# Optimization experiments

Hardware: AMD Instinct MI355X
Metric: run time of the kernel (lower is better)

Reference implementation:

```python
import jax, jax.numpy as jnp
import numpy as np

N = 10000           # nodes
E = 160000          # edges
MUL = 128           # multiplicity of each irrep (128x0e + 128x1o)
EDGE_FEAT = 8       # radial embedding dim
AVG_NUM_NEIGHBORS = 16.0
MLP_IN = MUL + MUL + EDGE_FEAT + 1  # 265
NUM_W = 4 * MUL     # irreps_mid num_irreps = 256x0e + 256x1o -> 512 path weights
SQ3 = float(np.sqrt(3.0))


def setup_inputs() -> dict:
    key = jax.random.key(0)
    ks = jax.random.split(key, 16)
    node_feats = jax.random.normal(ks[0], (N, 4 * MUL), dtype=jnp.float32)  # [N,512] = 128x0e ++ 128x1o
    edge_attrs = jax.random.normal(ks[1], (E, 4), dtype=jnp.float32)        # 1x0e ++ 1x1o
    edge_feats = jax.random.normal(ks[2], (E, EDGE_FEAT), dtype=jnp.float32)
    lengths = jax.random.uniform(ks[3], (E, 1), dtype=jnp.float32)
    edge_index = jax.random.randint(ks[4], (2, E), 0, N, dtype=jnp.int32)
    # e3nn Linear weights (stored unit-variance; forward applies 1/sqrt(fan_in))
    W_scalar = jax.random.normal(ks[5], (MUL, MUL), dtype=jnp.float32)
    W_up0 = jax.random.normal(ks[6], (MUL, MUL), dtype=jnp.float32)
    W_up1 = jax.random.normal(ks[7], (MUL, MUL), dtype=jnp.float32)
    # conv_tp_weights MLP (flax Dense: fan-scaled init, bias on first two layers)
    W1 = jax.random.normal(ks[8], (MLP_IN, MUL), dtype=jnp.float32) / np.sqrt(MLP_IN)
    b1 = jnp.zeros((MUL,), dtype=jnp.float32)
    W2 = jax.random.normal(ks[9], (MUL, MUL), dtype=jnp.float32) / np.sqrt(MUL)
    b2 = jnp.zeros((MUL,), dtype=jnp.float32)
    W3 = jax.random.normal(ks[10], (MUL, NUM_W), dtype=jnp.float32) / np.sqrt(MUL)
    # final e3nn Linear: 256x0e+256x1o -> 128x0e+128x1o
    Wout0 = jax.random.normal(ks[11], (2 * MUL, MUL), dtype=jnp.float32)
    Wout1 = jax.random.normal(ks[12], (2 * MUL, MUL), dtype=jnp.float32)
    return {"node_feats": node_feats, "edge_attrs": edge_attrs, "edge_feats": edge_feats,
            "lengths": lengths, "edge_index": edge_index, "W_scalar": W_scalar,
            "W_up0": W_up0, "W_up1": W_up1, "W1": W1, "b1": b1, "W2": W2, "b2": b2,
            "W3": W3, "Wout0": Wout0, "Wout1": Wout1}


def reference(node_feats, edge_attrs, edge_feats, lengths, edge_index,
              W_scalar, W_up0, W_up1, W1, b1, W2, b2, W3, Wout0, Wout1):
    n = node_feats.shape[0]
    inv = 1.0 / np.sqrt(MUL)
    x0 = node_feats[:, :MUL]                       # [N,128]   0e
    x1 = node_feats[:, MUL:].reshape(n, MUL, 3)    # [N,128,3] 1o

    # linear_scalar: only 0e->0e path survives
    scalars = (x0 @ W_scalar) * inv                # [N,128]
    # linear_up: per-irrep channel mixing
    h0 = (x0 @ W_up0) * inv                        # [N,128]
    h1 = jnp.einsum('nmi,mo->noi', x1, W_up1) * inv  # [N,128,3]

    sender, receiver = edge_index[0], edge_index[1]

    # conv_tp_weights MLP
    mlp_in = jnp.concatenate([scalars[sender], scalars[receiver], edge_feats, lengths], axis=-1)
    h = jax.nn.silu(mlp_in @ W1 + b1)
    h = jax.nn.silu(h @ W2 + b2)
    tpw = h @ W3                                   # [E,512]

    xs0 = h0[sender]                               # [E,128]
    xs1 = h1[sender]                               # [E,128,3]
    y0 = edge_attrs[:, 0:1]                        # [E,1]  0e
    y1 = edge_attrs[:, 1:4]                        # [E,3]  1o

    # CG tensor product (component normalization), filtered to {0e,1o}; sorted order:
    # 0e block = [0e*0e->0e, 1o*1o->0e], 1o block = [0e*1o->1o, 1o*0e->1o]
    mA = xs0 * y0                                       # [E,128]   0e
    mD = (xs1 * y1[:, None, :]).sum(-1) / SQ3           # [E,128]   0e
    mB = xs0[:, :, None] * y1[:, None, :]               # [E,128,3] 1o
    mC = xs1 * y0[:, :, None]                           # [E,128,3] 1o

    # per-irrep path weights (one scalar per irrep channel)
    wA, wD = tpw[:, :MUL], tpw[:, MUL:2 * MUL]
    wB, wC = tpw[:, 2 * MUL:3 * MUL], tpw[:, 3 * MUL:]

    m0 = jnp.concatenate([mA * wA, mD * wD], axis=1)                          # [E,256]
    m1 = jnp.concatenate([mB * wB[:, :, None], mC * wC[:, :, None]], axis=1)  # [E,256,3]

    # scatter-sum aggregation to receivers
    agg0 = jax.ops.segment_sum(m0, receiver, num_segments=n)  # [N,256]
    agg1 = jax.ops.segment_sum(m1, receiver, num_segments=n)  # [N,256,3]

    # final e3nn Linear + / avg_num_neighbors
    scale = 1.0 / (np.sqrt(2 * MUL) * AVG_NUM_NEIGHBORS)
    out0 = (agg0 @ Wout0) * scale                             # [N,128]
    out1 = jnp.einsum('nmi,mo->noi', agg1, Wout1) * scale     # [N,128,3]

    # reshape_irreps: [N, mul, sum(ir dims)] = [N,128,4]
    return jnp.concatenate([out0[:, :, None], out1], axis=-1)
```

## Files before the change

### kernel.cpp

```cpp
#include <hip/hip_runtime.h>
#include <hip/hip_bf16.h>

#define NN 10000
#define NE 160000
#define TILE 32
#define A1S 296
#define A2S 136

typedef __attribute__((ext_vector_type(8))) short short8;
typedef __attribute__((ext_vector_type(4))) float f32x4;

__device__ __forceinline__ float silu_f(float x) { return x / (1.0f + __expf(-x)); }
__device__ __forceinline__ unsigned short bf16u(float v) {
    __hip_bfloat16 b = __float2bfloat16(v);
    return *reinterpret_cast<unsigned short*>(&b);
}
__device__ __forceinline__ short8 pack8(float4 a, float4 b) {
    short8 r;
    r[0]=(short)bf16u(a.x); r[1]=(short)bf16u(a.y); r[2]=(short)bf16u(a.z); r[3]=(short)bf16u(a.w);
    r[4]=(short)bf16u(b.x); r[5]=(short)bf16u(b.y); r[6]=(short)bf16u(b.z); r[7]=(short)bf16u(b.w);
    return r;
}
__device__ __forceinline__ void lds_barrier() {
    asm volatile("s_waitcnt lgkmcnt(0)" ::: "memory");
    __builtin_amdgcn_s_barrier();
    asm volatile("" ::: "memory");
}

#define OFF_W1  0
#define OFF_W2  36864
#define OFF_W3  53248
#define OFF_WSC 118784
#define OFF_WU0 135168
#define OFF_WU1 151552
#define OFF_WO0 167936
#define OFF_WO1 200704
#define WP_TOTAL 233472

__global__ __launch_bounds__(256) void convert_weights(
    const float* __restrict__ W1, const float* __restrict__ W2,
    const float* __restrict__ W3, const float* __restrict__ Wsc,
    const float* __restrict__ Wu0, const float* __restrict__ Wu1,
    const float* __restrict__ Wo0, const float* __restrict__ Wo1,
    unsigned short* __restrict__ wp,
    const int* __restrict__ edge_index, int* __restrict__ deg)
{
    int idx = blockIdx.x * 256 + threadIdx.x;
    if (idx < NE) atomicAdd(&deg[edge_index[NE + idx]], 1);
    if (idx >= WP_TOTAL) return;
    const float* src; int off, N, K;
    if      (idx < OFF_W2)  { src = W1;  off = OFF_W1;  N = 128; K = 265; }
    else if (idx < OFF_W3)  { src = W2;  off = OFF_W2;  N = 128; K = 128; }
    else if (idx < OFF_WSC) { src = W3;  off = OFF_W3;  N = 512; K = 128; }
    else if (idx < OFF_WU0) { src = Wsc; off = OFF_WSC; N = 128; K = 128; }
    else if (idx < OFF_WU1) { src = Wu0; off = OFF_WU0; N = 128; K = 128; }
    else if (idx < OFF_WO0) { src = Wu1; off = OFF_WU1; N = 128; K = 128; }
    else if (idx < OFF_WO1) { src = Wo0; off = OFF_WO0; N = 128; K = 256; }
    else                    { src = Wo1; off = OFF_WO1; N = 128; K = 256; }
    int j = idx - off;
    int kt = j / (N * 32);
    int rem = j % (N * 32);
    int n = rem >> 5, kk = rem & 31;
    int k = kt * 32 + kk;
    wp[idx] = (k < K) ? bf16u(src[k * N + n]) : (unsigned short)0;
}

__global__ __launch_bounds__(256) void node_transform(
    const float* __restrict__ node_feats,
    const unsigned short* __restrict__ wp,
    unsigned short* __restrict__ scalars_bf,
    unsigned short* __restrict__ hall,
    float* __restrict__ agg0, float* __restrict__ agg1t)
{
    __shared__ unsigned short xls[4 * 16 * 136];
    const int t = threadIdx.x;
    const int bn = blockIdx.x * 16;

    {
        const float4 z = make_float4(0.f, 0.f, 0.f, 0.f);
        float4* a0 = (float4*)(agg0 + (size_t)bn * 256);
        #pragma unroll
        for (int i = 0; i < 4; ++i) a0[t + 256 * i] = z;
        #pragma unroll
        for (int c = 0; c < 3; ++c) {
            float4* a1 = (float4*)(agg1t + (size_t)c * NN * 256 + (size_t)bn * 256);
            #pragma unroll
            for (int i = 0; i < 4; ++i) a1[t + 256 * i] = z;
        }
    }

    for (int i = t; i < 16 * 512; i += 256) {
        int n = i >> 9, j = i & 511;
        unsigned short u = bf16u(node_feats[(size_t)(bn + n) * 512 + j]);
        if (j < 128) xls[n * 136 + j] = u;
        else {
            int jj = j - 128;
            int m = jj / 3;
            int c = jj - 3 * m;
            xls[(1 + c) * 2176 + n * 136 + m] = u;
        }
    }
    __syncthreads();

    const int wv = t >> 6, lane = t & 63, l16 = lane & 15, l4 = lane >> 4;
    const unsigned short* Wscp = wp + OFF_WSC;
    const unsigned short* Wu0p = wp + OFF_WU0;
    const unsigned short* Wu1p = wp + OFF_WU1;

    f32x4 asc[2] = {}, ah0[2] = {}, ah1[3][2] = {};
    for (int kt = 0; kt < 4; ++kt) {
        short8 ax0 = *(const short8*)(xls + l16 * 136 + kt * 32 + l4 * 8);
        short8 ax1[3];
        #pragma unroll
        for (int c = 0; c < 3; ++c)
            ax1[c] = *(const short8*)(xls + (1 + c) * 2176 + l16 * 136 + kt * 32 + l4 * 8);
        #pragma unroll
        for (int n = 0; n < 2; ++n) {
            int col = wv * 32 + n * 16 + l16;
            short8 bsc = *(const short8*)(Wscp + ((size_t)kt * 128 + col) * 32 + l4 * 8);
            short8 bu0 = *(const short8*)(Wu0p + ((size_t)kt * 128 + col) * 32 + l4 * 8);
            short8 bu1 = *(const short8*)(Wu1p + ((size_t)kt * 128 + col) * 32 + l4 * 8);
            asc[n] = __builtin_amdgcn_mfma_f32_16x16x32_bf16(ax0, bsc, asc[n], 0, 0, 0);
            ah0[n] = __builtin_amdgcn_mfma_f32_16x16x32_bf16(ax0, bu0, ah0[n], 0, 0, 0);
            #pragma unroll
            for (int c = 0; c < 3; ++c)
                ah1[c][n] = __builtin_amdgcn_mfma_f32_16x16x32_bf16(ax1[c], bu1, ah1[c][n], 0, 0, 0);
        }
    }
    const float inv = 0.08838834764831845f;
    #pragma unroll
    for (int n = 0; n < 2; ++n) {
        int col = wv * 32 + n * 16 + l16;
        #pragma unroll
        for (int r = 0; r < 4; ++r) {
            int node = bn + l4 * 4 + r;
            scalars_bf[(size_t)node * 128 + col] = bf16u(asc[n][r] * inv);
            unsigned int lo = (unsigned int)bf16u(ah0[n][r] * inv)
                            | ((unsigned int)bf16u(ah1[0][n][r] * inv) << 16);
            unsigned int hi = (unsigned int)bf16u(ah1[1][n][r] * inv)
                            | ((unsigned int)bf16u(ah1[2][n][r] * inv) << 16);
            *(uint2*)(hall + ((size_t)node * 128 + col) * 4) = make_uint2(lo, hi);
        }
    }
}

__global__ __launch_bounds__(1024) void scan_kernel(const int* __restrict__ deg,
                                                    int* __restrict__ cursor) {
    __shared__ int s[1024];
    const int t = threadIdx.x;
    const int base = t * 10;
    int ld[10];
    int lsum = 0;
    #pragma unroll
    for (int i = 0; i < 10; ++i) {
        int idx = base + i;
        ld[i] = (idx < NN) ? deg[idx] : 0;
        lsum += ld[i];
    }
    s[t] = lsum;
    __syncthreads();
    for (int off = 1; off < 1024; off <<= 1) {
        int u = (t >= off) ? s[t - off] : 0;
        __syncthreads();
        s[t] += u;
        __syncthreads();
    }
    int run = s[t] - lsum;
    #pragma unroll
    for (int i = 0; i < 10; ++i) {
        int idx = base + i;
        if (idx < NN) cursor[idx] = run;
        run += ld[i];
    }
}

__global__ __launch_bounds__(256) void perm_kernel(const int* __restrict__ edge_index,
                                                   int* __restrict__ cursor,
                                                   int* __restrict__ perm) {
    int e = blockIdx.x * 256 + threadIdx.x;
    if (e < NE) {
        int r = edge_index[NE + e];
        int pos = atomicAdd(&cursor[r], 1);
        perm[pos] = e;
    }
}

__global__ __launch_bounds__(256, 5) void edge_kernel(
    const unsigned short* __restrict__ scalars_bf,
    const unsigned short* __restrict__ hall,
    const float* __restrict__ edge_attrs,
    const float* __restrict__ edge_feats,
    const float* __restrict__ lengths,
    const int* __restrict__ edge_index,
    const int* __restrict__ perm,
    const float* __restrict__ b1, const float* __restrict__ b2,
    const unsigned short* __restrict__ wp,
    float* __restrict__ agg0, float* __restrict__ agg1t)
{
    __shared__ unsigned char smem_u[27648];
    __shared__ int   eid_s[TILE];
    __shared__ int   s_s[TILE];
    __shared__ int   r_s[TILE];
    __shared__ float4 y_s[TILE];

    unsigned short* A1 = (unsigned short*)smem_u;
    unsigned short* A2 = (unsigned short*)(smem_u + 18944);
    unsigned short* A3 = A1;
    float* PKh = (float*)(smem_u + 8704);

    const int t = threadIdx.x;
    const int e0 = blockIdx.x * TILE;
    const int wv = t >> 6;
    const int lane = t & 63;
    const int l16 = lane & 15;
    const int l4 = lane >> 4;

    if (t < TILE) {
        int eid = perm[e0 + t];
        eid_s[t] = eid;
        s_s[t] = edge_index[eid];
        r_s[t] = edge_index[NE + eid];
        y_s[t] = *(const float4*)(edge_attrs + (size_t)eid * 4);
    }
    __syncthreads();

    {
        const int e = t >> 3, j = t & 7;
        const unsigned short* srow = scalars_bf + (size_t)s_s[e] * 128;
        const unsigned short* rrow = scalars_bf + (size_t)r_s[e] * 128;
        *(uint4*)(A1 + e*A1S + j*16)       = *(const uint4*)(srow + j*16);
        *(uint4*)(A1 + e*A1S + j*16 + 8)   = *(const uint4*)(srow + j*16 + 8);
        *(uint4*)(A1 + e*A1S + 128 + j*16)     = *(const uint4*)(rrow + j*16);
        *(uint4*)(A1 + e*A1S + 128 + j*16 + 8) = *(const uint4*)(rrow + j*16 + 8);
        A1[e*A1S + 256 + j] = bf16u(edge_feats[(size_t)eid_s[e] * 8 + j]);
        if (t < TILE) A1[t*A1S + 264] = bf16u(lengths[eid_s[t]]);
        for (int i = t; i < TILE * 23; i += 256) {
            int row = i / 23, c = 265 + (i - row * 23);
            A1[row*A1S + c] = 0;
        }
    }

    const int q = t >> 6, o = t & 63;
    const int rlo = q * 8;
    uint2 pfA[8], pfB[8];
    #pragma unroll
    for (int i = 0; i < 8; ++i)
        pfA[i] = *(const uint2*)(hall + ((size_t)s_s[rlo + i] * 128 + o) * 4);
    __syncthreads();

    const unsigned short* Wp1 = wp + OFF_W1;
    const unsigned short* Wp2 = wp + OFF_W2;
    const unsigned short* Wp3 = wp + OFF_W3;

    {
        f32x4 acc[2][2] = {};
        for (int kt = 0; kt < 9; ++kt) {
            short8 a0 = *(const short8*)(A1 + (     l16)*A1S + kt*32 + l4*8);
            short8 a1 = *(const short8*)(A1 + (16 + l16)*A1S + kt*32 + l4*8);
            #pragma unroll
            for (int n = 0; n < 2; ++n) {
                int col = (2*wv + n)*16 + l16;
                short8 b = *(const short8*)(Wp1 + ((size_t)kt*128 + col)*32 + l4*8);
                acc[0][n] = __builtin_amdgcn_mfma_f32_16x16x32_bf16(a0, b, acc[0][n], 0, 0, 0);
                acc[1][n] = __builtin_amdgcn_mfma_f32_16x16x32_bf16(a1, b, acc[1][n], 0, 0, 0);
            }
        }
        #pragma unroll
        for (int n = 0; n < 2; ++n) {
            int col = (2*wv + n)*16 + l16;
            float bb = b1[col];
            #pragma unroll
            for (int m = 0; m < 2; ++m)
                #pragma unroll
                for (int r = 0; r < 4; ++r) {
                    int row = m*16 + l4*4 + r;
                    A2[row*A2S + col] = bf16u(silu_f(acc[m][n][r] + bb));
                }
        }
    }
    __syncthreads();

    {
        f32x4 acc[2][2] = {};
        for (int kt = 0; kt < 4; ++kt) {
            short8 a0 = *(const short8*)(A2 + (     l16)*A2S + kt*32 + l4*8);
            short8 a1 = *(const short8*)(A2 + (16 + l16)*A2S + kt*32 + l4*8);
            #pragma unroll
            for (int n = 0; n < 2; ++n) {
                int col = (2*wv + n)*16 + l16;
                short8 b = *(const short8*)(Wp2 + ((size_t)kt*128 + col)*32 + l4*8);
                acc[0][n] = __builtin_amdgcn_mfma_f32_16x16x32_bf16(a0, b, acc[0][n], 0, 0, 0);
                acc[1][n] = __builtin_amdgcn_mfma_f32_16x16x32_bf16(a1, b, acc[1][n], 0, 0, 0);
            }
        }
        #pragma unroll
        for (int n = 0; n < 2; ++n) {
            int col = (2*wv + n)*16 + l16;
            float bb = b2[col];
            #pragma unroll
            for (int m = 0; m < 2; ++m)
                #pragma unroll
                for (int r = 0; r < 4; ++r) {
                    int row = m*16 + l4*4 + r;
                    A3[row*A2S + col] = bf16u(silu_f(acc[m][n][r] + bb));
                }
        }
    }
    __syncthreads();

    const float rs3 = 0.57735026918962576f;
    auto do_seg = [&](const int pass, const int hh, const uint2* pf) {
        const int base0 = pass ? 128 : 0;
        const int base1 = pass ? 384 : 256;
        f32x4 acc[2][2] = {};
        for (int kt = 0; kt < 4; ++kt) {
            short8 a0 = *(const short8*)(A3 + (     l16)*A2S + kt*32 + l4*8);
            short8 a1 = *(const short8*)(A3 + (16 + l16)*A2S + kt*32 + l4*8);
            #pragma unroll
            for (int fam = 0; fam < 2; ++fam) {
                int col = (fam ? base1 : base0) + hh*64 + wv*16 + l16;
                short8 b = *(const short8*)(Wp3 + ((size_t)kt*512 + col)*32 + l4*8);
                acc[fam][0] = __builtin_amdgcn_mfma_f32_16x16x32_bf16(a0, b, acc[fam][0], 0, 0, 0);
                acc[fam][1] = __builtin_amdgcn_mfma_f32_16x16x32_bf16(a1, b, acc[fam][1], 0, 0, 0);
            }
        }
        #pragma unroll
        for (int fam = 0; fam < 2; ++fam)
            #pragma unroll
            for (int m = 0; m < 2; ++m)
                #pragma unroll
                for (int r = 0; r < 4; ++r) {
                    int row = m*16 + l4*4 + r;
                    float y0 = y_s[row].x;
                    float fold = (fam == 0) ? (pass ? rs3 : y0) : (pass ? y0 : 1.0f);
                    PKh[row*132 + fam*64 + wv*16 + l16] = acc[fam][m][r] * fold;
                }
        lds_barrier();

        {
            const int ocol = hh*64 + o;
            float ac0 = 0.f, ac1 = 0.f, ac2 = 0.f, ac3 = 0.f;
            int run_start = rlo;
            int prev_rn = r_s[rlo];

            auto flush = [&](int rn, bool interior) {
                size_t b0 = (size_t)rn * 256 + base0 + ocol;
                if (interior) {
                    agg0[b0] = ac0;
                    agg1t[0*(size_t)NN*256 + b0] = ac1;
                    agg1t[1*(size_t)NN*256 + b0] = ac2;
                    agg1t[2*(size_t)NN*256 + b0] = ac3;
                } else {
                    atomicAdd(agg0 + b0, ac0);
                    atomicAdd(agg1t + 0*(size_t)NN*256 + b0, ac1);
                    atomicAdd(agg1t + 1*(size_t)NN*256 + b0, ac2);
                    atomicAdd(agg1t + 2*(size_t)NN*256 + b0, ac3);
                }
            };

            #pragma unroll
            for (int i = 0; i < 8; ++i) {
                int row = rlo + i;
                int rn = r_s[row];
                if (rn != prev_rn) {
                    flush(prev_rn, run_start > rlo);
                    ac0 = ac1 = ac2 = ac3 = 0.f;
                    run_start = row;
                    prev_rn = rn;
                }
                float w0 = PKh[row*132 + o];
                float w1 = PKh[row*132 + 64 + o];
                float4 y = y_s[row];
                if (pass == 0) {
                    float x = __uint_as_float(pf[i].x << 16);
                    ac0 = fmaf(x, w0, ac0);
                    float xb = x * w1;
                    ac1 = fmaf(xb, y.y, ac1);
                    ac2 = fmaf(xb, y.z, ac2);
                    ac3 = fmaf(xb, y.w, ac3);
                } else {
                    float xx = __uint_as_float(pf[i].x & 0xffff0000u);
                    float xy = __uint_as_float(pf[i].y << 16);
                    float xz = __uint_as_float(pf[i].y & 0xffff0000u);
                    float dd = xx*y.y + xy*y.z + xz*y.w;
                    ac0 = fmaf(dd, w0, ac0);
                    ac1 = fmaf(xx, w1, ac1);
                    ac2 = fmaf(xy, w1, ac2);
                    ac3 = fmaf(xz, w1, ac3);
                }
            }
            flush(prev_rn, false);
        }
        lds_barrier();
    };

    do_seg(0, 0, pfA);
    do_seg(1, 0, pfA);
    #pragma unroll
    for (int i = 0; i < 8; ++i)
        pfB[i] = *(const uint2*)(hall + ((size_t)s_s[rlo + i] * 128 + 64 + o) * 4);
    do_seg(0, 1, pfB);
    do_seg(1, 1, pfB);
}

__global__ __launch_bounds__(256) void output_transform(
    const float* __restrict__ agg0,
    const float* __restrict__ agg1t,
    const unsigned short* __restrict__ wp,
    float* __restrict__ out)
{
    __shared__ unsigned short As[4][16 * 264];
    const int t = threadIdx.x;
    const int bn = blockIdx.x * 16;

    for (int i = t; i < 2048; i += 256) {
        int mat = i >> 9;
        int rem = i & 511;
        int n = rem >> 5;
        int ko = (rem & 31) * 8;
        const float* src = (mat == 0)
            ? (agg0 + (size_t)(bn + n) * 256 + ko)
            : (agg1t + (size_t)(mat - 1) * NN * 256 + (size_t)(bn + n) * 256 + ko);
        float4 v0 = *(const float4*)(src);
        float4 v1 = *(const float4*)(src + 4);
        *(short8*)(&As[mat][n * 264 + ko]) = pack8(v0, v1);
    }
    __syncthreads();

    const int wv = t >> 6, lane = t & 63, l16 = lane & 15, l4 = lane >> 4;
    const unsigned short* Wo0p = wp + OFF_WO0;
    const unsigned short* Wo1p = wp + OFF_WO1;

    f32x4 acc[2][4] = {};
    for (int kt = 0; kt < 8; ++kt) {
        short8 a0 = *(const short8*)(&As[0][l16 * 264 + kt * 32 + l4 * 8]);
        short8 a1 = *(const short8*)(&As[1][l16 * 264 + kt * 32 + l4 * 8]);
        short8 a2 = *(const short8*)(&As[2][l16 * 264 + kt * 32 + l4 * 8]);
        short8 a3 = *(const short8*)(&As[3][l16 * 264 + kt * 32 + l4 * 8]);
        #pragma unroll
        for (int n = 0; n < 2; ++n) {
            int col = wv * 32 + n * 16 + l16;
            short8 bw0 = *(const short8*)(Wo0p + ((size_t)kt * 128 + col) * 32 + l4 * 8);
            short8 bw1 = *(const short8*)(Wo1p + ((size_t)kt * 128 + col) * 32 + l4 * 8);
            acc[n][0] = __builtin_amdgcn_mfma_f32_16x16x32_bf16(a0, bw0, acc[n][0], 0, 0, 0);
            acc[n][1] = __builtin_amdgcn_mfma_f32_16x16x32_bf16(a1, bw1, acc[n][1], 0, 0, 0);
            acc[n][2] = __builtin_amdgcn_mfma_f32_16x16x32_bf16(a2, bw1, acc[n][2], 0, 0, 0);
            acc[n][3] = __builtin_amdgcn_mfma_f32_16x16x32_bf16(a3, bw1, acc[n][3], 0, 0, 0);
        }
    }
    const float scale = 0.00390625f;
    #pragma unroll
    for (int n = 0; n < 2; ++n) {
        int col = wv * 32 + n * 16 + l16;
        #pragma unroll
        for (int r = 0; r < 4; ++r) {
            int node = bn + l4 * 4 + r;
            float4 v = make_float4(acc[n][0][r] * scale, acc[n][1][r] * scale,
                                   acc[n][2][r] * scale, acc[n][3][r] * scale);
            *(float4*)(out + ((size_t)node * 128 + col) * 4) = v;
        }
    }
}

extern "C" void kernel_launch(void* const* d_in, const int* in_sizes, int n_in,
                              void* d_out, int out_size, void* d_ws, size_t ws_size,
                              hipStream_t stream) {
    const float* node_feats = (const float*)d_in[0];
    const float* edge_attrs = (const float*)d_in[1];
    const float* edge_feats = (const float*)d_in[2];
    const float* lengths    = (const float*)d_in[3];
    const int*   edge_index = (const int*)d_in[4];
    const float* W_scalar   = (const float*)d_in[5];
    const float* W_up0      = (const float*)d_in[6];
    const float* W_up1      = (const float*)d_in[7];
    const float* W1         = (const float*)d_in[8];
    const float* b1         = (const float*)d_in[9];
    const float* W2         = (const float*)d_in[10];
    const float* b2         = (const float*)d_in[11];
    const float* W3         = (const float*)d_in[12];
    const float* Wout0      = (const float*)d_in[13];
    const float* Wout1      = (const float*)d_in[14];

    float* ws = (float*)d_ws;
    unsigned short* scalars_bf = (unsigned short*)ws;
    unsigned short* hall = (unsigned short*)(ws + 640000);
    float* agg0  = ws + 3200000;
    float* agg1t = ws + 5760000;
    int* deg    = (int*)(ws + 13440000);
    int* cursor = (int*)(ws + 13450000);
    int* perm   = (int*)(ws + 13460000);
    unsigned short* wpack = (unsigned short*)(ws + 13620000);
    if (ws_size < 13736736ull * 4ull) return;

    hipMemsetAsync(deg, 0, NN * 4, stream);
    convert_weights<<<(WP_TOTAL + 255) / 256, 256, 0, stream>>>(
        W1, W2, W3, W_scalar, W_up0, W_up1, Wout0, Wout1, wpack, edge_index, deg);
    node_transform<<<625, 256, 0, stream>>>(node_feats, wpack, scalars_bf, hall, agg0, agg1t);
    scan_kernel<<<1, 1024, 0, stream>>>(deg, cursor);
    perm_kernel<<<(NE + 255) / 256, 256, 0, stream>>>(edge_index, cursor, perm);
    edge_kernel<<<NE / TILE, 256, 0, stream>>>(scalars_bf, hall, edge_attrs, edge_feats, lengths,
                                               edge_index, perm, b1, b2, wpack, agg0, agg1t);
    output_transform<<<625, 256, 0, stream>>>(agg0, agg1t, wpack, (float*)d_out);
}
```

Before: 201.4 us.

## Load first MLP layer A operands directly from global, drop A1 LDS staging

The first MLP GEMM now reads the gathered sender and receiver scalar rows and the edge features/lengths straight from global memory into MFMA A-fragments, instead of staging them through a padded LDS buffer. This removes the A1 buffer, one block barrier and the LDS write/read round trip, shrinks shared memory so occupancy can rise from 5 to 6 blocks, and replaces two __syncthreads with the lighter lds_barrier. In exchange each lane issues redundant uncoalesced global loads (rows reread by several waves), and the lighter barriers must still order A2/A3 reuse correctly.

```diff
diff --git a/kernel.cpp b/kernel.cpp
--- a/kernel.cpp
+++ b/kernel.cpp
@@ -4,7 +4,6 @@
 #define NN 10000
 #define NE 160000
 #define TILE 32
-#define A1S 296
 #define A2S 136
 
 typedef __attribute__((ext_vector_type(8))) short short8;
@@ -185,7 +184,7 @@
     }
 }
 
-__global__ __launch_bounds__(256, 5) void edge_kernel(
+__global__ __launch_bounds__(256, 6) void edge_kernel(
     const unsigned short* __restrict__ scalars_bf,
     const unsigned short* __restrict__ hall,
     const float* __restrict__ edge_attrs,
@@ -197,15 +196,14 @@
     const unsigned short* __restrict__ wp,
     float* __restrict__ agg0, float* __restrict__ agg1t)
 {
-    __shared__ unsigned char smem_u[27648];
+    __shared__ unsigned char smem_u[25600];
     __shared__ int   eid_s[TILE];
     __shared__ int   s_s[TILE];
     __shared__ int   r_s[TILE];
     __shared__ float4 y_s[TILE];
 
-    unsigned short* A1 = (unsigned short*)smem_u;
-    unsigned short* A2 = (unsigned short*)(smem_u + 18944);
-    unsigned short* A3 = A1;
+    unsigned short* A3 = (unsigned short*)smem_u;
+    unsigned short* A2 = (unsigned short*)(smem_u + 8704);
     float* PKh = (float*)(smem_u + 8704);
 
     const int t = threadIdx.x;
@@ -224,29 +222,12 @@
     }
     __syncthreads();
 
-    {
-        const int e = t >> 3, j = t & 7;
-        const unsigned short* srow = scalars_bf + (size_t)s_s[e] * 128;
-        const unsigned short* rrow = scalars_bf + (size_t)r_s[e] * 128;
-        *(uint4*)(A1 + e*A1S + j*16)       = *(const uint4*)(srow + j*16);
-        *(uint4*)(A1 + e*A1S + j*16 + 8)   = *(const uint4*)(srow + j*16 + 8);
-        *(uint4*)(A1 + e*A1S + 128 + j*16)     = *(const uint4*)(rrow + j*16);
-        *(uint4*)(A1 + e*A1S + 128 + j*16 + 8) = *(const uint4*)(rrow + j*16 + 8);
-        A1[e*A1S + 256 + j] = bf16u(edge_feats[(size_t)eid_s[e] * 8 + j]);
-        if (t < TILE) A1[t*A1S + 264] = bf16u(lengths[eid_s[t]]);
-        for (int i = t; i < TILE * 23; i += 256) {
-            int row = i / 23, c = 265 + (i - row * 23);
-            A1[row*A1S + c] = 0;
-        }
-    }
-
     const int q = t >> 6, o = t & 63;
     const int rlo = q * 8;
     uint2 pfA[8], pfB[8];
     #pragma unroll
     for (int i = 0; i < 8; ++i)
         pfA[i] = *(const uint2*)(hall + ((size_t)s_s[rlo + i] * 128 + o) * 4);
-    __syncthreads();
 
     const unsigned short* Wp1 = wp + OFF_W1;
     const unsigned short* Wp2 = wp + OFF_W2;
@@ -254,15 +235,56 @@
 
     {
         f32x4 acc[2][2] = {};
-        for (int kt = 0; kt < 9; ++kt) {
-            short8 a0 = *(const short8*)(A1 + (     l16)*A1S + kt*32 + l4*8);
-            short8 a1 = *(const short8*)(A1 + (16 + l16)*A1S + kt*32 + l4*8);
+        short8 ef0 = (short8){0,0,0,0,0,0,0,0}, ef1 = ef0;
+        {
+            int eA = l16, eB = 16 + l16;
+            if (l4 == 0) {
+                float4 v0 = *(const float4*)(edge_feats + (size_t)eid_s[eA] * 8);
+                float4 v1 = *(const float4*)(edge_feats + (size_t)eid_s[eA] * 8 + 4);
+                ef0 = pack8(v0, v1);
+                float4 u0 = *(const float4*)(edge_feats + (size_t)eid_s[eB] * 8);
+                float4 u1 = *(const float4*)(edge_feats + (size_t)eid_s[eB] * 8 + 4);
+                ef1 = pack8(u0, u1);
+            } else if (l4 == 1) {
+                ef0[0] = (short)bf16u(lengths[eid_s[eA]]);
+                ef1[0] = (short)bf16u(lengths[eid_s[eB]]);
+            }
+        }
+        const unsigned short* srowA = scalars_bf + (size_t)s_s[l16] * 128;
+        const unsigned short* srowB = scalars_bf + (size_t)s_s[16 + l16] * 128;
+        const unsigned short* rrowA = scalars_bf + (size_t)r_s[l16] * 128;
+        const unsigned short* rrowB = scalars_bf + (size_t)r_s[16 + l16] * 128;
+        #pragma unroll
+        for (int kt = 0; kt < 4; ++kt) {
+            short8 a0 = *(const short8*)(srowA + kt*32 + l4*8);
+            short8 a1 = *(const short8*)(srowB + kt*32 + l4*8);
             #pragma unroll
             for (int n = 0; n < 2; ++n) {
                 int col = (2*wv + n)*16 + l16;
                 short8 b = *(const short8*)(Wp1 + ((size_t)kt*128 + col)*32 + l4*8);
                 acc[0][n] = __builtin_amdgcn_mfma_f32_16x16x32_bf16(a0, b, acc[0][n], 0, 0, 0);
                 acc[1][n] = __builtin_amdgcn_mfma_f32_16x16x32_bf16(a1, b, acc[1][n], 0, 0, 0);
+            }
+        }
+        #pragma unroll
+        for (int kt = 4; kt < 8; ++kt) {
+            short8 a0 = *(const short8*)(rrowA + (kt-4)*32 + l4*8);
+            short8 a1 = *(const short8*)(rrowB + (kt-4)*32 + l4*8);
+            #pragma unroll
+            for (int n = 0; n < 2; ++n) {
+                int col = (2*wv + n)*16 + l16;
+                short8 b = *(const short8*)(Wp1 + ((size_t)kt*128 + col)*32 + l4*8);
+                acc[0][n] = __builtin_amdgcn_mfma_f32_16x16x32_bf16(a0, b, acc[0][n], 0, 0, 0);
+                acc[1][n] = __builtin_amdgcn_mfma_f32_16x16x32_bf16(a1, b, acc[1][n], 0, 0, 0);
+            }
+        }
+        {
+            #pragma unroll
+            for (int n = 0; n < 2; ++n) {
+                int col = (2*wv + n)*16 + l16;
+                short8 b = *(const short8*)(Wp1 + ((size_t)8*128 + col)*32 + l4*8);
+                acc[0][n] = __builtin_amdgcn_mfma_f32_16x16x32_bf16(ef0, b, acc[0][n], 0, 0, 0);
+                acc[1][n] = __builtin_amdgcn_mfma_f32_16x16x32_bf16(ef1, b, acc[1][n], 0, 0, 0);
             }
         }
         #pragma unroll
@@ -278,7 +300,7 @@
                 }
         }
     }
-    __syncthreads();
+    lds_barrier();
 
     {
         f32x4 acc[2][2] = {};
@@ -306,7 +328,7 @@
                 }
         }
     }
-    __syncthreads();
+    lds_barrier();
 
     const float rs3 = 0.57735026918962576f;
     auto do_seg = [&](const int pass, const int hh, const uint2* pf) {
```

Measured after the change: 235.3 us. +16.8%, slower.

## Double edge tile to 64 with 512-thread blocks and register-fed edge features

Applied to the files above, without the earlier changes.

The edge kernel now processes 64 edges per block with 8 waves instead of 32 edges with 4 waves. Each wave owns one 16-column slice of the MLP layers across all four row tiles, so each weight fragment loaded from global memory is reused across more edges. The final K-tile holding edge features and length is built directly in registers rather than staged through LDS with zero padding, which allows a narrower A1 stride. LDS use per block roughly doubles and the launch bounds change, which can lower occupancy and shift the balance of the scatter phase.

```diff
diff --git a/kernel.cpp b/kernel.cpp
--- a/kernel.cpp
+++ b/kernel.cpp
@@ -3,8 +3,8 @@
 
 #define NN 10000
 #define NE 160000
-#define TILE 32
-#define A1S 296
+#define TILE 64
+#define A1S 264
 #define A2S 136
 
 typedef __attribute__((ext_vector_type(8))) short short8;
@@ -185,7 +185,7 @@
     }
 }
 
-__global__ __launch_bounds__(256, 5) void edge_kernel(
+__global__ __launch_bounds__(512, 4) void edge_kernel(
     const unsigned short* __restrict__ scalars_bf,
     const unsigned short* __restrict__ hall,
     const float* __restrict__ edge_attrs,
@@ -197,16 +197,16 @@
     const unsigned short* __restrict__ wp,
     float* __restrict__ agg0, float* __restrict__ agg1t)
 {
-    __shared__ unsigned char smem_u[27648];
+    __shared__ unsigned char smem_u[51200];
     __shared__ int   eid_s[TILE];
     __shared__ int   s_s[TILE];
     __shared__ int   r_s[TILE];
     __shared__ float4 y_s[TILE];
 
     unsigned short* A1 = (unsigned short*)smem_u;
-    unsigned short* A2 = (unsigned short*)(smem_u + 18944);
+    unsigned short* A2 = (unsigned short*)(smem_u + 33792);
     unsigned short* A3 = A1;
-    float* PKh = (float*)(smem_u + 8704);
+    float* PKh = (float*)(smem_u + 17408);
 
     const int t = threadIdx.x;
     const int e0 = blockIdx.x * TILE;
@@ -214,6 +214,7 @@
     const int lane = t & 63;
     const int l16 = lane & 15;
     const int l4 = lane >> 4;
+    const int col = wv * 16 + l16;
 
     if (t < TILE) {
         int eid = perm[e0 + t];
@@ -232,15 +233,23 @@
         *(uint4*)(A1 + e*A1S + j*16 + 8)   = *(const uint4*)(srow + j*16 + 8);
         *(uint4*)(A1 + e*A1S + 128 + j*16)     = *(const uint4*)(rrow + j*16);
         *(uint4*)(A1 + e*A1S + 128 + j*16 + 8) = *(const uint4*)(rrow + j*16 + 8);
-        A1[e*A1S + 256 + j] = bf16u(edge_feats[(size_t)eid_s[e] * 8 + j]);
-        if (t < TILE) A1[t*A1S + 264] = bf16u(lengths[eid_s[t]]);
-        for (int i = t; i < TILE * 23; i += 256) {
-            int row = i / 23, c = 265 + (i - row * 23);
-            A1[row*A1S + c] = 0;
-        }
-    }
-
-    const int q = t >> 6, o = t & 63;
+    }
+
+    short8 ef[4];
+    #pragma unroll
+    for (int m = 0; m < 4; ++m) {
+        ef[m] = (short8){0,0,0,0,0,0,0,0};
+        int e = m*16 + l16;
+        if (l4 == 0) {
+            float4 v0 = *(const float4*)(edge_feats + (size_t)eid_s[e] * 8);
+            float4 v1 = *(const float4*)(edge_feats + (size_t)eid_s[e] * 8 + 4);
+            ef[m] = pack8(v0, v1);
+        } else if (l4 == 1) {
+            ef[m][0] = (short)bf16u(lengths[eid_s[e]]);
+        }
+    }
+
+    const int q = wv, o = lane;
     const int rlo = q * 8;
     uint2 pfA[8], pfB[8];
     #pragma unroll
@@ -253,73 +262,66 @@
     const unsigned short* Wp3 = wp + OFF_W3;
 
     {
-        f32x4 acc[2][2] = {};
-        for (int kt = 0; kt < 9; ++kt) {
-            short8 a0 = *(const short8*)(A1 + (     l16)*A1S + kt*32 + l4*8);
-            short8 a1 = *(const short8*)(A1 + (16 + l16)*A1S + kt*32 + l4*8);
-            #pragma unroll
-            for (int n = 0; n < 2; ++n) {
-                int col = (2*wv + n)*16 + l16;
-                short8 b = *(const short8*)(Wp1 + ((size_t)kt*128 + col)*32 + l4*8);
-                acc[0][n] = __builtin_amdgcn_mfma_f32_16x16x32_bf16(a0, b, acc[0][n], 0, 0, 0);
-                acc[1][n] = __builtin_amdgcn_mfma_f32_16x16x32_bf16(a1, b, acc[1][n], 0, 0, 0);
+        f32x4 acc[4] = {};
+        for (int kt = 0; kt < 8; ++kt) {
+            short8 b = *(const short8*)(Wp1 + ((size_t)kt*128 + col)*32 + l4*8);
+            #pragma unroll
+            for (int m = 0; m < 4; ++m) {
+                short8 a = *(const short8*)(A1 + (m*16 + l16)*A1S + kt*32 + l4*8);
+                acc[m] = __builtin_amdgcn_mfma_f32_16x16x32_bf16(a, b, acc[m], 0, 0, 0);
             }
         }
-        #pragma unroll
-        for (int n = 0; n < 2; ++n) {
-            int col = (2*wv + n)*16 + l16;
-            float bb = b1[col];
-            #pragma unroll
-            for (int m = 0; m < 2; ++m)
-                #pragma unroll
-                for (int r = 0; r < 4; ++r) {
-                    int row = m*16 + l4*4 + r;
-                    A2[row*A2S + col] = bf16u(silu_f(acc[m][n][r] + bb));
-                }
-        }
+        {
+            short8 b = *(const short8*)(Wp1 + ((size_t)8*128 + col)*32 + l4*8);
+            #pragma unroll
+            for (int m = 0; m < 4; ++m)
+                acc[m] = __builtin_amdgcn_mfma_f32_16x16x32_bf16(ef[m], b, acc[m], 0, 0, 0);
+        }
+        float bb = b1[col];
+        #pragma unroll
+        for (int m = 0; m < 4; ++m)
+            #pragma unroll
+            for (int r = 0; r < 4; ++r) {
+                int row = m*16 + l4*4 + r;
+                A2[row*A2S + col] = bf16u(silu_f(acc[m][r] + bb));
+            }
     }
     __syncthreads();
 
     {
-        f32x4 acc[2][2] = {};
+        f32x4 acc[4] = {};
         for (int kt = 0; kt < 4; ++kt) {
-            short8 a0 = *(const short8*)(A2 + (     l16)*A2S + kt*32 + l4*8);
-            short8 a1 = *(const short8*)(A2 + (16 + l16)*A2S + kt*32 + l4*8);
-            #pragma unroll
-            for (int n = 0; n < 2; ++n) {
-                int col = (2*wv + n)*16 + l16;
-                short8 b = *(const short8*)(Wp2 + ((size_t)kt*128 + col)*32 + l4*8);
-                acc[0][n] = __builtin_amdgcn_mfma_f32_16x16x32_bf16(a0, b, acc[0][n], 0, 0, 0);
-                acc[1][n] = __builtin_amdgcn_mfma_f32_16x16x32_bf16(a1, b, acc[1][n], 0, 0, 0);
+            short8 b = *(const short8*)(Wp2 + ((size_t)kt*128 + col)*32 + l4*8);
+            #pragma unroll
+            for (int m = 0; m < 4; ++m) {
+                short8 a = *(const short8*)(A2 + (m*16 + l16)*A2S + kt*32 + l4*8);
+                acc[m] = __builtin_amdgcn_mfma_f32_16x16x32_bf16(a, b, acc[m], 0, 0, 0);
             }
         }
-        #pragma unroll
-        for (int n = 0; n < 2; ++n) {
-            int col = (2*wv + n)*16 + l16;
-            float bb = b2[col];
-            #pragma unroll
-            for (int m = 0; m < 2; ++m)
-                #pragma unroll
-                for (int r = 0; r < 4; ++r) {
-                    int row = m*16 + l4*4 + r;
-                    A3[row*A2S + col] = bf16u(silu_f(acc[m][n][r] + bb));
-                }
-        }
-    }
-    __syncthreads();
-
+        float bb = b2[col];
+        #pragma unroll
+        for (int m = 0; m < 4; ++m)
+            #pragma unroll
+            for (int r = 0; r < 4; ++r) {
+                int row = m*16 + l4*4 + r;
+                A3[row*A2S + col] = bf16u(silu_f(acc[m][r] + bb));
+            }
+    }
+    __syncthreads();
+
+    const int cw = wv & 3, mh = wv >> 2;
     const float rs3 = 0.57735026918962576f;
     auto do_seg = [&](const int pass, const int hh, const uint2* pf) {
         const int base0 = pass ? 128 : 0;
         const int base1 = pass ? 384 : 256;
         f32x4 acc[2][2] = {};
         for (int kt = 0; kt < 4; ++kt) {
-            short8 a0 = *(const short8*)(A3 + (     l16)*A2S + kt*32 + l4*8);
-            short8 a1 = *(const short8*)(A3 + (16 + l16)*A2S + kt*32 + l4*8);
+            short8 a0 = *(const short8*)(A3 + (mh*32 +      l16)*A2S + kt*32 + l4*8);
+            short8 a1 = *(const short8*)(A3 + (mh*32 + 16 + l16)*A2S + kt*32 + l4*8);
             #pragma unroll
             for (int fam = 0; fam < 2; ++fam) {
-                int col = (fam ? base1 : base0) + hh*64 + wv*16 + l16;
-                short8 b = *(const short8*)(Wp3 + ((size_t)kt*512 + col)*32 + l4*8);
+                int c3 = (fam ? base1 : base0) + hh*64 + cw*16 + l16;
+                short8 b = *(const short8*)(Wp3 + ((size_t)kt*512 + c3)*32 + l4*8);
                 acc[fam][0] = __builtin_amdgcn_mfma_f32_16x16x32_bf16(a0, b, acc[fam][0], 0, 0, 0);
                 acc[fam][1] = __builtin_amdgcn_mfma_f32_16x16x32_bf16(a1, b, acc[fam][1], 0, 0, 0);
             }
@@ -330,10 +332,10 @@
             for (int m = 0; m < 2; ++m)
                 #pragma unroll
                 for (int r = 0; r < 4; ++r) {
-                    int row = m*16 + l4*4 + r;
+                    int row = mh*32 + m*16 + l4*4 + r;
                     float y0 = y_s[row].x;
                     float fold = (fam == 0) ? (pass ? rs3 : y0) : (pass ? y0 : 1.0f);
-                    PKh[row*132 + fam*64 + wv*16 + l16] = acc[fam][m][r] * fold;
+                    PKh[row*132 + fam*64 + cw*16 + l16] = acc[fam][m][r] * fold;
                 }
         lds_barrier();
 
@@ -498,7 +500,7 @@
     node_transform<<<625, 256, 0, stream>>>(node_feats, wpack, scalars_bf, hall, agg0, agg1t);
     scan_kernel<<<1, 1024, 0, stream>>>(deg, cursor);
     perm_kernel<<<(NE + 255) / 256, 256, 0, stream>>>(edge_index, cursor, perm);
-    edge_kernel<<<NE / TILE, 256, 0, stream>>>(scalars_bf, hall, edge_attrs, edge_feats, lengths,
+    edge_kernel<<<NE / TILE, 512, 0, stream>>>(scalars_bf, hall, edge_attrs, edge_feats, lengths,
                                                edge_index, perm, b1, b2, wpack, agg0, agg1t);
     output_transform<<<625, 256, 0, stream>>>(agg0, agg1t, wpack, (float*)d_out);
 }
```

Result: slower. 215.2 us (+6.9%).
